# Kernel optimization log

Measured on AMD Instinct MI355X. Metric: run time of the kernel, lower is better.

## Reference

```python
import jax, jax.numpy as jnp
import numpy as np

D = 1024      # embedding_dim
H = 16        # n_heads
HD = D // H   # head_dim = 64
E = 8         # num_experts
K = 2         # top_k
I = 1024      # moe intermediate
S = 2048      # seq_len
B = 1
EPS = 1e-6
THETA = 10000.0


def _rmsnorm(x, w):
    xf = x.astype(jnp.float32)
    var = jnp.mean(xf * xf, axis=-1, keepdims=True)
    return (xf * jax.lax.rsqrt(var + EPS)).astype(x.dtype) * w


def _rope(x, positions):
    # x: [B, S, H, HD], neox-style rotate-half RoPE
    half = HD // 2
    inv_freq = 1.0 / (THETA ** (jnp.arange(0, half, dtype=jnp.float32) / half))
    freqs = positions.astype(jnp.float32)[:, None] * inv_freq[None, :]  # [S, half]
    cos = jnp.cos(freqs)[None, :, None, :]
    sin = jnp.sin(freqs)[None, :, None, :]
    x1, x2 = x[..., :half], x[..., half:]
    return jnp.concatenate([x1 * cos - x2 * sin, x1 * sin + x2 * cos], axis=-1).astype(x.dtype)


def _attn(x, positions, wqkv, wo):
    b, s, _ = x.shape
    qkv = (x @ wqkv).reshape(b, s, 3, H, HD)
    q, k, v = qkv[:, :, 0], qkv[:, :, 1], qkv[:, :, 2]
    q = _rope(q, positions)
    k = _rope(k, positions)
    scale = 1.0 / np.sqrt(HD)
    scores = jnp.einsum('bqhd,bkhd->bhqk', q, k) * scale
    causal = jnp.tril(jnp.ones((s, s), dtype=bool))
    scores = jnp.where(causal[None, None], scores, jnp.finfo(scores.dtype).min)
    probs = jax.nn.softmax(scores, axis=-1)
    o = jnp.einsum('bhqk,bkhd->bqhd', probs, v).reshape(b, s, D)
    return o @ wo


def _moe(x, gate_w, wg, wu, wd):
    # x: [T, D]
    T = x.shape[0]
    logits = x @ gate_w                                    # [T, E]
    probs = jax.nn.softmax(logits.astype(jnp.float32), axis=-1)
    vals, idx = jax.lax.top_k(probs, K)                    # [T, K]
    vals = vals / jnp.sum(vals, axis=-1, keepdims=True)    # renormalize=True
    combine = jnp.zeros((T, E), dtype=jnp.float32)
    combine = combine.at[jnp.arange(T)[:, None], idx].add(vals)
    combine = combine.astype(x.dtype)                      # [T, E]
    out = jnp.zeros_like(x)
    for e in range(E):  # fixed small expert loop; SwiGLU expert FFN
        h = jax.nn.silu(x @ wg[e]) * (x @ wu[e])
        out = out + combine[:, e:e + 1] * (h @ wd[e])
    return out


def setup_inputs() -> dict:
    key = jax.random.key(0)
    ks = jax.random.split(key, 8)
    std = 0.02
    return {
        'positions': jnp.arange(S, dtype=jnp.int32),
        'hidden_states': jax.random.normal(ks[0], (B, S, D), jnp.float32),
        'residual': jax.random.normal(ks[1], (B, S, D), jnp.float32),
        'ln1_w': jnp.ones((D,), jnp.float32),
        'ln2_w': jnp.ones((D,), jnp.float32),
        'wqkv': jax.random.normal(ks[2], (D, 3 * D), jnp.float32) * std,
        'wo': jax.random.normal(ks[3], (D, D), jnp.float32) * std,
        'gate_w': jax.random.normal(ks[4], (D, E), jnp.float32) * std,
        'wg': jax.random.normal(ks[5], (E, D, I), jnp.float32) * std,
        'wu': jax.random.normal(ks[6], (E, D, I), jnp.float32) * std,
        'wd': jax.random.normal(ks[7], (E, I, D), jnp.float32) * std,
    }


def reference(positions, hidden_states, residual, ln1_w, ln2_w, wqkv, wo, gate_w, wg, wu, wd):
    # _forward_with_post_attn_norm: residual arg is overwritten by hidden_states
    res = hidden_states
    x = _rmsnorm(hidden_states, ln1_w)
    x = res + _attn(x, positions, wqkv, wo)
    res2 = x
    y = _rmsnorm(x, ln2_w)
    b, s, _ = y.shape
    moe_out = _moe(y.reshape(-1, D), gate_w, wg, wu, wd).reshape(b, s, D)
    return res2 + moe_out
```

## Files before the change

### kernel.cpp

```cpp
#include <hip/hip_runtime.h>
#include <math.h>

constexpr int S  = 2048;
constexpr int D  = 1024;
constexpr int NH = 16;
constexpr int NE = 8;
constexpr float EPS   = 1e-6f;
constexpr float THETA = 10000.0f;
constexpr float SCL2  = 0.125f * 1.4426950408889634f;
constexpr float LOG2E = 1.4426950408889634f;

typedef unsigned short u16;
typedef unsigned int   u32;
typedef unsigned long long u64;
typedef __attribute__((ext_vector_type(8))) short short8;
typedef __attribute__((ext_vector_type(4))) float f32x4;

__device__ __forceinline__ u16 f2bf(float x) {
  union { float f; u32 u; } v; v.f = x;
  u32 r = (v.u + 0x7FFFu + ((v.u >> 16) & 1u)) >> 16;
  return (u16)r;
}
__device__ __forceinline__ float bf2f(u16 h) {
  union { u32 u; float f; } v; v.u = ((u32)h) << 16;
  return v.f;
}
__device__ __forceinline__ f32x4 mfma16(short8 a, short8 b, f32x4 c) {
  return __builtin_amdgcn_mfma_f32_16x16x32_bf16(a, b, c, 0, 0, 0);
}
__device__ __forceinline__ void gl_lds16(const void* g, void* l) {
  __builtin_amdgcn_global_load_lds((const __attribute__((address_space(1))) u32*)g,
                                   (__attribute__((address_space(3))) u32*)l, 16, 0, 0);
}
__device__ __forceinline__ u64 pack4bf(float a, float b, float c, float d) {
  return (u64)f2bf(a) | ((u64)f2bf(b) << 16) | ((u64)f2bf(c) << 32) | ((u64)f2bf(d) << 48);
}

__global__ __launch_bounds__(256) void prep_kernel(const float* __restrict__ wqkv,
    const float* __restrict__ wo, const float* __restrict__ wg, const float* __restrict__ wu,
    const float* __restrict__ wd, const int* __restrict__ positions,
    const float* __restrict__ hidden, const float* __restrict__ ln1_w,
    u16* __restrict__ wqkvT2, u16* __restrict__ woT2, u16* __restrict__ wgT,
    u16* __restrict__ wuT, u16* __restrict__ wdT, float2* __restrict__ ropetab,
    u16* __restrict__ xn2, int* __restrict__ counts) {
  const int b = blockIdx.x;
  const int tid = threadIdx.x;
  if (b >= 7424) {
    const int t = b - 7424;
    const float* xr = hidden + (size_t)t * D;
    float v[4]; float ss = 0.f;
#pragma unroll
    for (int i = 0; i < 4; ++i) { v[i] = xr[tid + i * 256]; ss += v[i] * v[i]; }
#pragma unroll
    for (int m = 32; m >= 1; m >>= 1) ss += __shfl_xor(ss, m, 64);
    __shared__ float red[4];
    if ((tid & 63) == 0) red[tid >> 6] = ss;
    __syncthreads();
    const float rs = rsqrtf((red[0] + red[1] + red[2] + red[3]) * (1.f / (float)D) + EPS);
#pragma unroll
    for (int i = 0; i < 4; ++i) {
      const int d = tid + i * 256;
      const float y = v[i] * rs * ln1_w[d];
      const u16 h = f2bf(y);
      xn2[(size_t)t * 2048 + d] = h;
      xn2[(size_t)t * 2048 + 1024 + d] = f2bf(y - bf2f(h));
    }
    return;
  }
  if (b >= 7168) {
    if (b == 7168 && tid < 8) counts[tid] = 0;
    const int idx = (b - 7168) * 256 + tid;
    const int t = idx >> 5, p = idx & 31;
    const float inv = powf(THETA, -(float)p * (1.f / 32.f));
    const float fr = (float)positions[t] * inv;
    float sn, cs; sincosf(fr, &sn, &cs);
    ropetab[idx] = make_float2(cs, sn);
    return;
  }
  __shared__ float t_[64][65];
  const float* W; u16* out; int N, n0, k0; bool split;
  if (b < 768) {
    W = wqkv; out = wqkvT2; N = 3072; split = true;
    n0 = (b % 48) * 64; k0 = (b / 48) * 64;
  } else if (b < 1024) {
    W = wo; out = woT2; N = 1024; split = true;
    const int r = b - 768; n0 = (r & 15) * 64; k0 = (r >> 4) * 64;
  } else {
    int r;
    if (b < 3072)      { r = b - 1024; const int e = r >> 8; W = wg + (size_t)e * 1048576; out = wgT + (size_t)e * 1048576; }
    else if (b < 5120) { r = b - 3072; const int e = r >> 8; W = wu + (size_t)e * 1048576; out = wuT + (size_t)e * 1048576; }
    else               { r = b - 5120; const int e = r >> 8; W = wd + (size_t)e * 1048576; out = wdT + (size_t)e * 1048576; }
    N = 1024; split = false;
    r &= 255; n0 = (r & 15) * 64; k0 = (r >> 4) * 64;
  }
  const int rr = tid >> 4, c4 = (tid & 15) * 4;
#pragma unroll
  for (int i = 0; i < 4; ++i) {
    const float4 v = *(const float4*)(W + (size_t)(k0 + rr + i * 16) * N + n0 + c4);
    t_[rr + i * 16][c4 + 0] = v.x; t_[rr + i * 16][c4 + 1] = v.y;
    t_[rr + i * 16][c4 + 2] = v.z; t_[rr + i * 16][c4 + 3] = v.w;
  }
  __syncthreads();
  if (split) {
#pragma unroll
    for (int i = 0; i < 4; ++i) {
      const int n = n0 + rr + i * 16;
      u16* oh = out + (size_t)n * 2048 + k0 + c4;
      const float v0 = t_[c4 + 0][rr + i * 16], v1 = t_[c4 + 1][rr + i * 16];
      const float v2 = t_[c4 + 2][rr + i * 16], v3 = t_[c4 + 3][rr + i * 16];
      *(u64*)(void*)oh = pack4bf(v0, v1, v2, v3);
      *(u64*)(void*)(oh + 1024) = pack4bf(v0 - bf2f(f2bf(v0)), v1 - bf2f(f2bf(v1)),
                                          v2 - bf2f(f2bf(v2)), v3 - bf2f(f2bf(v3)));
    }
  } else {
#pragma unroll
    for (int i = 0; i < 4; ++i) {
      const int n = n0 + rr + i * 16;
      u16* o = out + (size_t)n * 1024 + k0 + c4;
      *(u64*)(void*)o = pack4bf(t_[c4 + 0][rr + i * 16], t_[c4 + 1][rr + i * 16],
                                t_[c4 + 2][rr + i * 16], t_[c4 + 3][rr + i * 16]);
    }
  }
}

__global__ __launch_bounds__(256) void gemm_qkv(const u16* __restrict__ A2,
    const u16* __restrict__ Bt2, float* __restrict__ Cpart) {
  __shared__ u16 As[2][128 * 32];
  __shared__ u16 Bs[2][128 * 32];
  const int b = blockIdx.x;
  const int xcd = b & 7, ii = b >> 3;
  const int m0 = (ii & 15) * 128;
  const int np = (ii >> 4) % 3, ks = (ii >> 4) / 3;
  const int n0 = (xcd * 3 + np) * 128;
  const int kk0 = ks * 48, kk1 = kk0 + 48;
  const int tid = threadIdx.x, wv = tid >> 6, lane = tid & 63;
  const int l15 = lane & 15, lg = lane >> 4;
  const int wr = wv >> 1, wc = wv & 1;
  const int sr = lane >> 2, sk = (lane & 3) * 16;
  const u16* aptr[2]; const u16* bptr[2];
#pragma unroll
  for (int i = 0; i < 2; ++i) {
    aptr[i] = A2 + (size_t)(m0 + (wv * 2 + i) * 16 + sr) * 2048;
    bptr[i] = Bt2 + (size_t)(n0 + (wv * 2 + i) * 16 + sr) * 2048;
  }
  auto STAGE = [&](int buf, int kk) {
    const int t = kk * 32;
    int ka, kb;
    if (t < 1024)      { ka = t;        kb = t; }
    else if (t < 2048) { ka = t;        kb = t - 1024; }
    else               { ka = t - 2048; kb = t - 1024; }
#pragma unroll
    for (int i = 0; i < 2; ++i) {
      gl_lds16((const char*)(aptr[i] + ka) + sk, (char*)As + buf * 8192 + (wv * 2 + i) * 1024);
      gl_lds16((const char*)(bptr[i] + kb) + sk, (char*)Bs + buf * 8192 + (wv * 2 + i) * 1024);
    }
  };
  f32x4 acc[4][4] = {};
  STAGE(0, kk0);
  __syncthreads();
  int cur = 0;
  for (int kk = kk0; kk < kk1; ++kk) {
    if (kk + 1 < kk1) STAGE(cur ^ 1, kk + 1);
    const u16* Ab = (const u16*)As + cur * 4096;
    const u16* Bb = (const u16*)Bs + cur * 4096;
    short8 a[4], bb[4];
#pragma unroll
    for (int i = 0; i < 4; ++i)
      a[i] = *(const short8*)(const void*)(Ab + (size_t)(wr * 64 + i * 16 + l15) * 32 + lg * 8);
#pragma unroll
    for (int j = 0; j < 4; ++j)
      bb[j] = *(const short8*)(const void*)(Bb + (size_t)(wc * 64 + j * 16 + l15) * 32 + lg * 8);
    __builtin_amdgcn_s_setprio(1);
#pragma unroll
    for (int i = 0; i < 4; ++i)
#pragma unroll
      for (int j = 0; j < 4; ++j) acc[i][j] = mfma16(a[i], bb[j], acc[i][j]);
    __builtin_amdgcn_s_setprio(0);
    __syncthreads();
    cur ^= 1;
  }
  float* P = Cpart + (size_t)ks * S * 3072;
#pragma unroll
  for (int i = 0; i < 4; ++i)
#pragma unroll
    for (int j = 0; j < 4; ++j)
#pragma unroll
      for (int r = 0; r < 4; ++r) {
        const int row = m0 + wr * 64 + i * 16 + lg * 4 + r;
        const int col = n0 + wc * 64 + j * 16 + l15;
        P[(size_t)row * 3072 + col] = acc[i][j][r];
      }
}

__global__ __launch_bounds__(256) void qkv_combine(const float* __restrict__ Cp,
    const float2* __restrict__ tab, u16* __restrict__ Ch, u16* __restrict__ Cl) {
  const int t = blockIdx.x, tid = threadIdx.x;
  const float* r0 = Cp + (size_t)t * 3072;
  const float* r1 = r0 + (size_t)S * 3072;
  const size_t ob = (size_t)t * 3072;
#pragma unroll
  for (int i = 0; i < 4; ++i) {
    const int pi = tid + i * 256;
    const int h = pi >> 5, p = pi & 31;
    const int col = h * 64 + p;
    const float x1 = r0[col] + r1[col];
    const float x2 = r0[col + 32] + r1[col + 32];
    const float2 cs = tab[t * 32 + p];
    const float y1 = x1 * cs.x - x2 * cs.y;
    const float y2 = x1 * cs.y + x2 * cs.x;
    const u16 h1 = f2bf(y1);
    Ch[ob + col] = h1; Cl[ob + col] = f2bf(y1 - bf2f(h1));
    const u16 h2 = f2bf(y2);
    Ch[ob + col + 32] = h2; Cl[ob + col + 32] = f2bf(y2 - bf2f(h2));
  }
#pragma unroll
  for (int i = 0; i < 4; ++i) {
    const int col = 2048 + tid + i * 256;
    const float y = r0[col] + r1[col];
    const u16 h = f2bf(y);
    Ch[ob + col] = h; Cl[ob + col] = f2bf(y - bf2f(h));
  }
}

__global__ __launch_bounds__(256) void gemm_wo(const u16* __restrict__ A2,
    const u16* __restrict__ Bt2, float* __restrict__ Pout) {
  constexpr int N = 1024;
  __shared__ u16 As[2][128 * 32];
  __shared__ u16 Bs[2][128 * 32];
  const int b = blockIdx.x;
  const int xcd = b & 7, ii = b >> 3;
  const int n0 = xcd * 128;
  const int m0 = (ii & 15) * 128;
  const int ks = ii >> 4;
  const int kk0 = ks * 24, kk1 = kk0 + 24;
  const int tid = threadIdx.x, wv = tid >> 6, lane = tid & 63;
  const int l15 = lane & 15, lg = lane >> 4;
  const int wr = wv >> 1, wc = wv & 1;
  const int sr = lane >> 2, sk = (lane & 3) * 16;
  const u16* aptr[2]; const u16* bptr[2];
#pragma unroll
  for (int i = 0; i < 2; ++i) {
    aptr[i] = A2 + (size_t)(m0 + (wv * 2 + i) * 16 + sr) * 2048;
    bptr[i] = Bt2 + (size_t)(n0 + (wv * 2 + i) * 16 + sr) * 2048;
  }
  auto STAGE = [&](int buf, int kk) {
    const int t = kk * 32;
    int ka, kb;
    if (t < 1024)      { ka = t;        kb = t; }
    else if (t < 2048) { ka = t;        kb = t - 1024; }
    else               { ka = t - 2048; kb = t - 1024; }
#pragma unroll
    for (int i = 0; i < 2; ++i) {
      gl_lds16((const char*)(aptr[i] + ka) + sk, (char*)As + buf * 8192 + (wv * 2 + i) * 1024);
      gl_lds16((const char*)(bptr[i] + kb) + sk, (char*)Bs + buf * 8192 + (wv * 2 + i) * 1024);
    }
  };
  f32x4 acc[4][4] = {};
  STAGE(0, kk0);
  __syncthreads();
  int cur = 0;
  for (int kk = kk0; kk < kk1; ++kk) {
    if (kk + 1 < kk1) STAGE(cur ^ 1, kk + 1);
    const u16* Ab = (const u16*)As + cur * 4096;
    const u16* Bb = (const u16*)Bs + cur * 4096;
    short8 a[4], bb[4];
#pragma unroll
    for (int i = 0; i < 4; ++i)
      a[i] = *(const short8*)(const void*)(Ab + (size_t)(wr * 64 + i * 16 + l15) * 32 + lg * 8);
#pragma unroll
    for (int j = 0; j < 4; ++j)
      bb[j] = *(const short8*)(const void*)(Bb + (size_t)(wc * 64 + j * 16 + l15) * 32 + lg * 8);
    __builtin_amdgcn_s_setprio(1);
#pragma unroll
    for (int i = 0; i < 4; ++i)
#pragma unroll
      for (int j = 0; j < 4; ++j) acc[i][j] = mfma16(a[i], bb[j], acc[i][j]);
    __builtin_amdgcn_s_setprio(0);
    __syncthreads();
    cur ^= 1;
  }
  float* P = Pout + (size_t)ks * S * N;
#pragma unroll
  for (int i = 0; i < 4; ++i)
#pragma unroll
    for (int j = 0; j < 4; ++j)
#pragma unroll
      for (int r = 0; r < 4; ++r) {
        const int row = m0 + wr * 64 + i * 16 + lg * 4 + r;
        const int col = n0 + wc * 64 + j * 16 + l15;
        P[(size_t)row * N + col] = acc[i][j][r];
      }
}

__global__ __launch_bounds__(256) void attn_mfma(const u16* __restrict__ Qh,
    const u16* __restrict__ Ql, float* __restrict__ Opart, float2* __restrict__ ml) {
  const int b = blockIdx.x;
  const int head = (b & 7) + 8 * ((b >> 3) & 1);
  const int qb = 31 - ((b >> 4) & 31);
  const int sp = (b >> 9) & 3;
  const int q0 = qb * 64;
  const int ktiles = qb + 1;
  const int kbase = ktiles >> 2, krem = ktiles & 3;
  const int t0 = sp * kbase + (sp < krem ? sp : krem);
  const int t1 = t0 + kbase + (sp < krem ? 1 : 0);
  const int tid = threadIdx.x, w = tid >> 6, lane = tid & 63;
  const int l15 = lane & 15, lg = lane >> 4;
  __shared__ u16 Kh[64 * 64];
  __shared__ u16 Kl[64 * 64];
  __shared__ __align__(16) u16 Vth[64 * 72];
  __shared__ __align__(16) u16 Vtl[64 * 72];
  __shared__ u32 Pp[4][16 * 68];

  short8 qh[2], qlo[2];
  {
    const size_t qbase = (size_t)(q0 + w * 16 + l15) * 3072 + head * 64;
    qh[0]  = *(const short8*)(const void*)(Qh + qbase + lg * 8);
    qh[1]  = *(const short8*)(const void*)(Qh + qbase + 32 + lg * 8);
    qlo[0] = *(const short8*)(const void*)(Ql + qbase + lg * 8);
    qlo[1] = *(const short8*)(const void*)(Ql + qbase + 32 + lg * 8);
  }
  f32x4 oacc[4] = {};
  float m_run[4], l_run[4];
#pragma unroll
  for (int r = 0; r < 4; ++r) { m_run[r] = -__builtin_inff(); l_run[r] = 0.f; }
  const int qrow0 = q0 + w * 16 + lg * 4;

  const int vhl = tid >> 7, rem = tid & 127;
  const int vkq = rem & 15, vdg = rem >> 4;
  const u16* vbase = (vhl ? Ql : Qh) + 2048 + head * 64 + vdg * 8;
  u16* vdst = vhl ? Vtl : Vth;
  short8 vr[4];

  auto STAGEK = [&](int kt) {
#pragma unroll
    for (int i = 0; i < 2; ++i) {
      const int inst = w * 2 + i;
      const int key = inst * 8 + (lane >> 3);
      const int db = ((lane & 7) * 16) ^ ((key & 7) << 4);
      gl_lds16((const char*)(Qh + (size_t)(kt * 64 + key) * 3072 + 1024 + head * 64) + db,
               (char*)Kh + inst * 1024);
      gl_lds16((const char*)(Ql + (size_t)(kt * 64 + key) * 3072 + 1024 + head * 64) + db,
               (char*)Kl + inst * 1024);
    }
  };
  auto VLOAD = [&](int kt) {
    const u16* vs = vbase + (size_t)(kt * 64 + vkq * 4) * 3072;
    vr[0] = *(const short8*)(const void*)vs;
    vr[1] = *(const short8*)(const void*)(vs + 3072);
    vr[2] = *(const short8*)(const void*)(vs + 6144);
    vr[3] = *(const short8*)(const void*)(vs + 9216);
  };
  auto VWRITE = [&]() {
#pragma unroll
    for (int jj = 0; jj < 8; ++jj) {
      const u64 pk = (u64)(u16)vr[0][jj] | ((u64)(u16)vr[1][jj] << 16) |
                     ((u64)(u16)vr[2][jj] << 32) | ((u64)(u16)vr[3][jj] << 48);
      *(u64*)(void*)(vdst + (vdg * 8 + jj) * 72 + vkq * 4) = pk;
    }
  };

  if (t0 < t1) {
    STAGEK(t0);
    VLOAD(t0);
    VWRITE();
    __syncthreads();
  }
  for (int t = t0; t < t1; ++t) {
    const int k0 = t * 64;
    const bool more = (t + 1 < t1);
    f32x4 sacc[4];
    __builtin_amdgcn_s_setprio(1);
#pragma unroll
    for (int nt = 0; nt < 4; ++nt) {
      const int key = nt * 16 + l15;
      const char* kbh = (const char*)Kh + key * 128;
      const char* kbl = (const char*)Kl + key * 128;
      const int sw = (key & 7) << 4;
      const short8 kh0 = *(const short8*)(const void*)(kbh + ((lg * 16) ^ sw));
      const short8 kh1 = *(const short8*)(const void*)(kbh + ((64 + lg * 16) ^ sw));
      const short8 kl0 = *(const short8*)(const void*)(kbl + ((lg * 16) ^ sw));
      const short8 kl1 = *(const short8*)(const void*)(kbl + ((64 + lg * 16) ^ sw));
      f32x4 s = {};
      s = mfma16(qh[0], kh0, s); s = mfma16(qh[1], kh1, s);
      s = mfma16(qlo[0], kh0, s); s = mfma16(qlo[1], kh1, s);
      s = mfma16(qh[0], kl0, s); s = mfma16(qh[1], kl1, s);
      sacc[nt] = s;
    }
    __builtin_amdgcn_s_setprio(0);
    __syncthreads();
    if (more) { STAGEK(t + 1); VLOAD(t + 1); }
#pragma unroll
    for (int nt = 0; nt < 4; ++nt)
#pragma unroll
      for (int r = 0; r < 4; ++r) sacc[nt][r] *= SCL2;
    if (t == qb) {
#pragma unroll
      for (int nt = 0; nt < 4; ++nt) {
        const int key = k0 + nt * 16 + l15;
#pragma unroll
        for (int r = 0; r < 4; ++r)
          if (key > qrow0 + r) sacc[nt][r] = -__builtin_inff();
      }
    }
    float mx4[4];
#pragma unroll
    for (int r = 0; r < 4; ++r) {
      float mx = fmaxf(fmaxf(sacc[0][r], sacc[1][r]), fmaxf(sacc[2][r], sacc[3][r]));
#pragma unroll
      for (int msk = 8; msk >= 1; msk >>= 1) mx = fmaxf(mx, __shfl_xor(mx, msk, 64));
      mx4[r] = mx;
    }
    const bool grow = (mx4[0] > m_run[0] + 8.f) || (mx4[1] > m_run[1] + 8.f) ||
                      (mx4[2] > m_run[2] + 8.f) || (mx4[3] > m_run[3] + 8.f);
    if (__any(grow)) {
#pragma unroll
      for (int r = 0; r < 4; ++r) {
        const float m_new = fmaxf(m_run[r], mx4[r]);
        const float fac = __builtin_amdgcn_exp2f(m_run[r] - m_new);
        m_run[r] = m_new;
        l_run[r] *= fac;
#pragma unroll
        for (int nd = 0; nd < 4; ++nd) oacc[nd][r] *= fac;
      }
    }
#pragma unroll
    for (int nt = 0; nt < 4; ++nt)
#pragma unroll
      for (int r = 0; r < 4; ++r)
        sacc[nt][r] = __builtin_amdgcn_exp2f(sacc[nt][r] - m_run[r]);
#pragma unroll
    for (int r = 0; r < 4; ++r) {
      float ls = sacc[0][r] + sacc[1][r] + sacc[2][r] + sacc[3][r];
#pragma unroll
      for (int msk = 8; msk >= 1; msk >>= 1) ls += __shfl_xor(ls, msk, 64);
      l_run[r] += ls;
    }
#pragma unroll
    for (int nt = 0; nt < 4; ++nt)
#pragma unroll
      for (int r = 0; r < 4; ++r) {
        const float p = sacc[nt][r];
        const u32 xu = __float_as_uint(p);
        const u32 hi = xu & 0xFFFF0000u;
        const float pl = p - __uint_as_float(hi);
        const u32 lw = __float_as_uint(pl) >> 16;
        Pp[w][(lg * 4 + r) * 68 + nt * 16 + l15] = (xu >> 16) | (lw << 16);
      }
    __builtin_amdgcn_s_setprio(1);
#pragma unroll
    for (int kk2 = 0; kk2 < 2; ++kk2) {
      const u32* prow = &Pp[w][l15 * 68 + kk2 * 32 + lg * 8];
      const uint4 pq0 = *(const uint4*)prow;
      const uint4 pq1 = *(const uint4*)(prow + 4);
      union U8 { u32 wd[4]; short8 v; } ph_, pl_;
      ph_.wd[0] = (pq0.x & 0xFFFFu) | (pq0.y << 16);
      ph_.wd[1] = (pq0.z & 0xFFFFu) | (pq0.w << 16);
      ph_.wd[2] = (pq1.x & 0xFFFFu) | (pq1.y << 16);
      ph_.wd[3] = (pq1.z & 0xFFFFu) | (pq1.w << 16);
      pl_.wd[0] = (pq0.x >> 16) | (pq0.y & 0xFFFF0000u);
      pl_.wd[1] = (pq0.z >> 16) | (pq0.w & 0xFFFF0000u);
      pl_.wd[2] = (pq1.x >> 16) | (pq1.y & 0xFFFF0000u);
      pl_.wd[3] = (pq1.z >> 16) | (pq1.w & 0xFFFF0000u);
#pragma unroll
      for (int nd = 0; nd < 4; ++nd) {
        const short8 vbh = *(const short8*)(const void*)((const char*)Vth + (nd * 16 + l15) * 144 + kk2 * 64 + lg * 16);
        const short8 vbl = *(const short8*)(const void*)((const char*)Vtl + (nd * 16 + l15) * 144 + kk2 * 64 + lg * 16);
        oacc[nd] = mfma16(ph_.v, vbh, oacc[nd]);
        oacc[nd] = mfma16(pl_.v, vbh, oacc[nd]);
        oacc[nd] = mfma16(ph_.v, vbl, oacc[nd]);
      }
    }
    __builtin_amdgcn_s_setprio(0);
    __syncthreads();
    if (more) VWRITE();
  }
  float* Op = Opart + (size_t)sp * S * 1024;
#pragma unroll
  for (int nd = 0; nd < 4; ++nd)
#pragma unroll
    for (int r = 0; r < 4; ++r)
      Op[(size_t)(qrow0 + r) * 1024 + head * 64 + nd * 16 + l15] = oacc[nd][r];
  if (l15 == 0) {
#pragma unroll
    for (int r = 0; r < 4; ++r)
      ml[((size_t)sp * S + qrow0 + r) * NH + head] = make_float2(m_run[r], l_run[r]);
  }
}

__global__ __launch_bounds__(256) void attn_combine(const float* __restrict__ Op,
    const float2* __restrict__ ml, u16* __restrict__ OA2) {
  const int t = blockIdx.x, tid = threadIdx.x;
  const int h = tid >> 4, dq = (tid & 15) * 4;
  float2 a[4];
  float M = -__builtin_inff();
#pragma unroll
  for (int c = 0; c < 4; ++c) {
    a[c] = ml[((size_t)c * S + t) * NH + h];
    if (a[c].y > 0.f) M = fmaxf(M, a[c].x);
  }
  float e[4], denom = 0.f;
#pragma unroll
  for (int c = 0; c < 4; ++c) {
    e[c] = (a[c].y > 0.f) ? exp2f(a[c].x - M) : 0.f;
    denom += e[c] * a[c].y;
  }
  const float inv = 1.f / denom;
  float ov[4] = {0.f, 0.f, 0.f, 0.f};
#pragma unroll
  for (int c = 0; c < 4; ++c) {
    const float4 v = *(const float4*)(Op + ((size_t)c * S + t) * 1024 + h * 64 + dq);
    ov[0] += e[c] * v.x; ov[1] += e[c] * v.y; ov[2] += e[c] * v.z; ov[3] += e[c] * v.w;
  }
#pragma unroll
  for (int c2 = 0; c2 < 4; ++c2) {
    const float o = ov[c2] * inv;
    const size_t idx = (size_t)t * 2048 + h * 64 + dq + c2;
    const u16 hb = f2bf(o);
    OA2[idx] = hb;
    OA2[idx + 1024] = f2bf(o - bf2f(hb));
  }
}

__global__ __launch_bounds__(256) void rmsnorm_res2_gate(const float* __restrict__ hidden,
    const float* __restrict__ p01, const float* __restrict__ w2, const float* __restrict__ GW,
    float* __restrict__ out, u16* __restrict__ yb,
    int* __restrict__ counts, int* __restrict__ tok_map, float* __restrict__ w_map) {
  const int t = blockIdx.x;
  float v[4]; float ss = 0.f;
#pragma unroll
  for (int i = 0; i < 4; ++i) {
    const size_t idx = (size_t)t * D + threadIdx.x + i * 256;
    const float r = hidden[idx] + p01[idx] + p01[idx + (size_t)S * D] +
                    p01[idx + 2 * (size_t)S * D] + p01[idx + 3 * (size_t)S * D];
    v[i] = r; ss += r * r;
  }
#pragma unroll
  for (int m = 32; m >= 1; m >>= 1) ss += __shfl_xor(ss, m, 64);
  __shared__ float red[4];
  if ((threadIdx.x & 63) == 0) red[threadIdx.x >> 6] = ss;
  __syncthreads();
  const float rs = rsqrtf((red[0] + red[1] + red[2] + red[3]) * (1.f / (float)D) + EPS);
  float lg[8] = {};
#pragma unroll
  for (int i = 0; i < 4; ++i) {
    const int d = threadIdx.x + i * 256;
    const size_t idx = (size_t)t * D + d;
    const float y = v[i] * rs * w2[d];
    out[idx] = v[i];
    yb[idx] = f2bf(y);
    const float4 g0 = *(const float4*)(GW + d * 8);
    const float4 g1 = *(const float4*)(GW + d * 8 + 4);
    lg[0] += y * g0.x; lg[1] += y * g0.y; lg[2] += y * g0.z; lg[3] += y * g0.w;
    lg[4] += y * g1.x; lg[5] += y * g1.y; lg[6] += y * g1.z; lg[7] += y * g1.w;
  }
#pragma unroll
  for (int e = 0; e < 8; ++e)
#pragma unroll
    for (int m = 32; m >= 1; m >>= 1) lg[e] += __shfl_xor(lg[e], m, 64);
  __shared__ float wred[4][8];
  if ((threadIdx.x & 63) == 0)
#pragma unroll
    for (int e = 0; e < 8; ++e) wred[threadIdx.x >> 6][e] = lg[e];
  __syncthreads();
  if (threadIdx.x == 0) {
    float L[8];
#pragma unroll
    for (int e = 0; e < 8; ++e) L[e] = wred[0][e] + wred[1][e] + wred[2][e] + wred[3][e];
    int i0 = 0; float v0 = L[0];
    for (int i = 1; i < 8; ++i) if (L[i] > v0) { v0 = L[i]; i0 = i; }
    int i1 = -1; float v1 = -__builtin_inff();
    for (int i = 0; i < 8; ++i) if (i != i0 && L[i] > v1) { v1 = L[i]; i1 = i; }
    const float e1 = expf(v1 - v0);
    const float inv = 1.f / (1.f + e1);
    const int p0 = atomicAdd(&counts[i0], 1);
    tok_map[i0 * S + p0] = t;
    w_map[i0 * S + p0] = inv;
    const int p1 = atomicAdd(&counts[i1], 1);
    tok_map[i1 * S + p1] = t | 65536;
    w_map[i1 * S + p1] = e1 * inv;
  }
}

__global__ __launch_bounds__(256) void moe_gu(const u16* __restrict__ Yb,
    const u16* __restrict__ Wgb, const u16* __restrict__ Wub, u16* __restrict__ Hb,
    const int* __restrict__ counts, const int* __restrict__ tokmap) {
  const int b = blockIdx.x;
  const int e = b & 7, ii = b >> 3;
  const int n0 = (ii & 15) * 64;
  const int m0 = (ii >> 4) * 128;
  const int cnt = counts[e];
  if (m0 >= cnt) return;
  __shared__ u16 SH[2][16 * 512];
  const int tid = threadIdx.x, wv = tid >> 6, lane = tid & 63;
  const int l15 = lane & 15, lg = lane >> 4;
  const int wr = wv >> 1, wc = wv & 1;
  const int sr = lane >> 2, sk = (lane & 3) * 16;
  const u16* B1 = Wgb + (size_t)e * 1048576;
  const u16* B2 = Wub + (size_t)e * 1048576;
  const u16* cp[4];
#pragma unroll
  for (int i = 0; i < 4; ++i) {
    const int c = wv * 4 + i;
    if (c < 8) {
      const int arow = m0 + c * 16 + sr;
      const int tok = tokmap[e * S + arow] & 2047;
      cp[i] = Yb + (size_t)tok * 1024;
    } else if (c < 12) {
      cp[i] = B1 + (size_t)(n0 + (c - 8) * 16 + sr) * 1024;
    } else {
      cp[i] = B2 + (size_t)(n0 + (c - 12) * 16 + sr) * 1024;
    }
  }
  auto STAGE = [&](int buf, int k) {
#pragma unroll
    for (int i = 0; i < 4; ++i) {
      const int c = wv * 4 + i;
      gl_lds16((const char*)(cp[i] + k) + sk, (char*)SH + buf * 16384 + c * 1024);
    }
  };
  f32x4 acc1[4][2] = {};
  f32x4 acc2[4][2] = {};
  STAGE(0, 0);
  __syncthreads();
  int cur = 0;
  for (int kk = 0; kk < 32; ++kk) {
    if (kk < 31) STAGE(cur ^ 1, (kk + 1) * 32);
    const u16* Sb = (const u16*)SH + cur * 8192;
    short8 a[4], b1f[2], b2f[2];
#pragma unroll
    for (int i = 0; i < 4; ++i)
      a[i] = *(const short8*)(const void*)(Sb + (size_t)(wr * 64 + i * 16 + l15) * 32 + lg * 8);
#pragma unroll
    for (int j = 0; j < 2; ++j) {
      b1f[j] = *(const short8*)(const void*)(Sb + 4096 + (size_t)(wc * 32 + j * 16 + l15) * 32 + lg * 8);
      b2f[j] = *(const short8*)(const void*)(Sb + 6144 + (size_t)(wc * 32 + j * 16 + l15) * 32 + lg * 8);
    }
    __builtin_amdgcn_s_setprio(1);
#pragma unroll
    for (int i = 0; i < 4; ++i)
#pragma unroll
      for (int j = 0; j < 2; ++j) {
        acc1[i][j] = mfma16(a[i], b1f[j], acc1[i][j]);
        acc2[i][j] = mfma16(a[i], b2f[j], acc2[i][j]);
      }
    __builtin_amdgcn_s_setprio(0);
    __syncthreads();
    cur ^= 1;
  }
#pragma unroll
  for (int i = 0; i < 4; ++i)
#pragma unroll
    for (int j = 0; j < 2; ++j)
#pragma unroll
      for (int r = 0; r < 4; ++r) {
        const int row = m0 + wr * 64 + i * 16 + lg * 4 + r;
        if (row < cnt) {
          const float g = acc1[i][j][r];
          const float u = acc2[i][j][r];
          const float sig = __builtin_amdgcn_rcpf(1.f + __builtin_amdgcn_exp2f(-g * LOG2E));
          Hb[((size_t)e * 2048 + row) * 1024 + n0 + wc * 32 + j * 16 + l15] = f2bf(u * g * sig);
        }
      }
}

__global__ __launch_bounds__(256) void moe_down(const u16* __restrict__ Hb,
    const u16* __restrict__ Wdb, u16* __restrict__ slotp,
    const int* __restrict__ counts, const int* __restrict__ tokmap,
    const float* __restrict__ wmap) {
  const int b = blockIdx.x;
  const int e = b & 7, ii = b >> 3;
  const int m0 = (ii & 15) * 128;
  const int n0 = ((ii >> 4) & 7) * 128;
  const int ks = ii >> 7;
  const int cnt = counts[e];
  if (m0 >= cnt) return;
  __shared__ u16 As[2][128 * 32];
  __shared__ u16 Bs[2][128 * 32];
  const int tid = threadIdx.x, wv = tid >> 6, lane = tid & 63;
  const int l15 = lane & 15, lg = lane >> 4;
  const int wr = wv >> 1, wc = wv & 1;
  const int sr = lane >> 2, sk = (lane & 3) * 16;
  const u16* B = Wdb + (size_t)e * 1048576;
  const u16* aptr[2]; const u16* bptr[2];
#pragma unroll
  for (int i = 0; i < 2; ++i) {
    aptr[i] = Hb + ((size_t)e * 2048 + m0 + (wv * 2 + i) * 16 + sr) * 1024;
    bptr[i] = B + (size_t)(n0 + (wv * 2 + i) * 16 + sr) * 1024;
  }
  auto STAGE = [&](int buf, int k) {
#pragma unroll
    for (int i = 0; i < 2; ++i) {
      gl_lds16((const char*)(aptr[i] + k) + sk, (char*)As + buf * 8192 + (wv * 2 + i) * 1024);
      gl_lds16((const char*)(bptr[i] + k) + sk, (char*)Bs + buf * 8192 + (wv * 2 + i) * 1024);
    }
  };
  f32x4 acc[4][4] = {};
  const int kb0 = ks * 16, kb1 = kb0 + 16;
  STAGE(0, kb0 * 32);
  __syncthreads();
  int cur = 0;
  for (int kk = kb0; kk < kb1; ++kk) {
    if (kk + 1 < kb1) STAGE(cur ^ 1, (kk + 1) * 32);
    const u16* Ab = (const u16*)As + cur * 4096;
    const u16* Bb = (const u16*)Bs + cur * 4096;
    short8 a[4], bb[4];
#pragma unroll
    for (int i = 0; i < 4; ++i)
      a[i] = *(const short8*)(const void*)(Ab + (size_t)(wr * 64 + i * 16 + l15) * 32 + lg * 8);
#pragma unroll
    for (int j = 0; j < 4; ++j)
      bb[j] = *(const short8*)(const void*)(Bb + (size_t)(wc * 64 + j * 16 + l15) * 32 + lg * 8);
    __builtin_amdgcn_s_setprio(1);
#pragma unroll
    for (int i = 0; i < 4; ++i)
#pragma unroll
      for (int j = 0; j < 4; ++j) acc[i][j] = mfma16(a[i], bb[j], acc[i][j]);
    __builtin_amdgcn_s_setprio(0);
    __syncthreads();
    cur ^= 1;
  }
#pragma unroll
  for (int i = 0; i < 4; ++i)
#pragma unroll
    for (int j = 0; j < 4; ++j)
#pragma unroll
      for (int r = 0; r < 4; ++r) {
        const int row = m0 + wr * 64 + i * 16 + lg * 4 + r;
        if (row < cnt) {
          const int raw = tokmap[e * S + row];
          const int t = raw & 2047;
          const int sl = (raw >> 16) & 1;
          const float wgt = wmap[e * S + row];
          slotp[((size_t)(sl * 2 + ks) * S + t) * 1024 + n0 + wc * 64 + j * 16 + l15] =
              f2bf(wgt * acc[i][j][r]);
        }
      }
}

__global__ __launch_bounds__(256) void final_add(float* __restrict__ out,
    const u16* __restrict__ sp) {
  const size_t i = ((size_t)blockIdx.x * 256 + threadIdx.x) * 4;
  float4 o = *(float4*)(out + i);
#pragma unroll
  for (int c = 0; c < 4; ++c) {
    const u64 a = *(const u64*)(sp + (size_t)c * S * D + i);
    o.x += bf2f((u16)(a));
    o.y += bf2f((u16)(a >> 16));
    o.z += bf2f((u16)(a >> 32));
    o.w += bf2f((u16)(a >> 48));
  }
  *(float4*)(out + i) = o;
}

extern "C" void kernel_launch(void* const* d_in, const int* in_sizes, int n_in,
                              void* d_out, int out_size, void* d_ws, size_t ws_size,
                              hipStream_t stream) {
  const int*   positions = (const int*)d_in[0];
  const float* hidden    = (const float*)d_in[1];
  const float* ln1_w  = (const float*)d_in[3];
  const float* ln2_w  = (const float*)d_in[4];
  const float* wqkv   = (const float*)d_in[5];
  const float* wo     = (const float*)d_in[6];
  const float* gate_w = (const float*)d_in[7];
  const float* wg     = (const float*)d_in[8];
  const float* wu     = (const float*)d_in[9];
  const float* wd     = (const float*)d_in[10];
  float* out = (float*)d_out;

  char* ws = (char*)d_ws;
  const size_t MB = 1ull << 20;
  u16* wqkvT2 = (u16*)(ws);
  u16* QKVh   = (u16*)(ws);
  u16* OA2    = (u16*)(ws);
  u16* woT2   = (u16*)(ws + 12 * MB);
  u16* wgT    = (u16*)(ws + 16 * MB);
  u16* wuT    = (u16*)(ws + 32 * MB);
  u16* wdT    = (u16*)(ws + 48 * MB);
  float2* ropetab = (float2*)(ws + 64 * MB);
  float2* ml      = (float2*)(ws + 64 * MB + 524288);
  char* mapb = ws + 64 * MB + 1572864;
  int*   counts   = (int*)mapb;
  int*   tok_map  = (int*)(mapb + 8192);
  float* w_map    = (float*)(mapb + 8192 + 65536);
  u16* xn2    = (u16*)(ws + 66 * MB);
  u16* QKVl   = (u16*)(ws + 66 * MB);
  u16* yb     = (u16*)(ws + 66 * MB);
  float* Cpart  = (float*)(ws + 78 * MB);
  float* Opart  = (float*)(ws + 78 * MB);
  float* p01    = (float*)(ws + 78 * MB);
  u16* Hb     = (u16*)(ws + 78 * MB);
  u16* slotp  = (u16*)(ws + 110 * MB);

  prep_kernel<<<9472, 256, 0, stream>>>(wqkv, wo, wg, wu, wd, positions, hidden, ln1_w,
                                        wqkvT2, woT2, wgT, wuT, wdT, ropetab, xn2, counts);
  gemm_qkv<<<768, 256, 0, stream>>>(xn2, wqkvT2, Cpart);
  qkv_combine<<<S, 256, 0, stream>>>(Cpart, ropetab, QKVh, QKVl);
  attn_mfma<<<2048, 256, 0, stream>>>(QKVh, QKVl, Opart, ml);
  attn_combine<<<S, 256, 0, stream>>>(Opart, ml, OA2);
  gemm_wo<<<512, 256, 0, stream>>>(OA2, woT2, p01);
  rmsnorm_res2_gate<<<S, 256, 0, stream>>>(hidden, p01, ln2_w, gate_w, out, yb,
                                           counts, tok_map, w_map);
  moe_gu<<<2048, 256, 0, stream>>>(yb, wgT, wuT, Hb, counts, tok_map);
  moe_down<<<2048, 256, 0, stream>>>(Hb, wdT, slotp, counts, tok_map, w_map);
  final_add<<<2048, 256, 0, stream>>>(out, slotp);
}
```

Before: 315.7 us.

## Transpose attention score MFMA so each lane owns one query row

The QK^T MFMA now uses K as the A operand and Q as B, so each lane holds a single query's scores. Row max and sum then need only two cross-lane shuffles, and the running max and sum shrink to scalars. The Kl tile is no longer staged in LDS; it is read directly from global memory into registers each tile. P is written to LDS as bf16 hi, then rewritten as the lo part for a second PV pass, with launch bounds set to 4 blocks. This is meant to cut shuffle work and LDS footprint, at the cost of uncoalesced global Kl loads and an extra LDS write/read round for P.

```diff
diff --git a/kernel.cpp b/kernel.cpp
--- a/kernel.cpp
+++ b/kernel.cpp
@@ -292,7 +292,7 @@
       }
 }
 
-__global__ __launch_bounds__(256) void attn_mfma(const u16* __restrict__ Qh,
+__global__ __launch_bounds__(256, 4) void attn_mfma(const u16* __restrict__ Qh,
     const u16* __restrict__ Ql, float* __restrict__ Opart, float2* __restrict__ ml) {
   const int b = blockIdx.x;
   const int head = (b & 7) + 8 * ((b >> 3) & 1);
@@ -306,10 +306,9 @@
   const int tid = threadIdx.x, w = tid >> 6, lane = tid & 63;
   const int l15 = lane & 15, lg = lane >> 4;
   __shared__ u16 Kh[64 * 64];
-  __shared__ u16 Kl[64 * 64];
   __shared__ __align__(16) u16 Vth[64 * 72];
   __shared__ __align__(16) u16 Vtl[64 * 72];
-  __shared__ u32 Pp[4][16 * 68];
+  __shared__ __align__(16) u16 Pp[4][16 * 72];
 
   short8 qh[2], qlo[2];
   {
@@ -320,10 +319,9 @@
     qlo[1] = *(const short8*)(const void*)(Ql + qbase + 32 + lg * 8);
   }
   f32x4 oacc[4] = {};
-  float m_run[4], l_run[4];
-#pragma unroll
-  for (int r = 0; r < 4; ++r) { m_run[r] = -__builtin_inff(); l_run[r] = 0.f; }
+  float m_run = -__builtin_inff(), l_run = 0.f;
   const int qrow0 = q0 + w * 16 + lg * 4;
+  const int qcol  = q0 + w * 16 + l15;
 
   const int vhl = tid >> 7, rem = tid & 127;
   const int vkq = rem & 15, vdg = rem >> 4;
@@ -339,8 +337,6 @@
       const int db = ((lane & 7) * 16) ^ ((key & 7) << 4);
       gl_lds16((const char*)(Qh + (size_t)(kt * 64 + key) * 3072 + 1024 + head * 64) + db,
                (char*)Kh + inst * 1024);
-      gl_lds16((const char*)(Ql + (size_t)(kt * 64 + key) * 3072 + 1024 + head * 64) + db,
-               (char*)Kl + inst * 1024);
     }
   };
   auto VLOAD = [&](int kt) {
@@ -368,22 +364,26 @@
   for (int t = t0; t < t1; ++t) {
     const int k0 = t * 64;
     const bool more = (t + 1 < t1);
+    short8 kl[8];
+#pragma unroll
+    for (int nt = 0; nt < 4; ++nt) {
+      const u16* ksrc = Ql + (size_t)(k0 + nt * 16 + l15) * 3072 + 1024 + head * 64 + lg * 8;
+      kl[nt * 2]     = *(const short8*)(const void*)ksrc;
+      kl[nt * 2 + 1] = *(const short8*)(const void*)(ksrc + 32);
+    }
     f32x4 sacc[4];
     __builtin_amdgcn_s_setprio(1);
 #pragma unroll
     for (int nt = 0; nt < 4; ++nt) {
       const int key = nt * 16 + l15;
       const char* kbh = (const char*)Kh + key * 128;
-      const char* kbl = (const char*)Kl + key * 128;
       const int sw = (key & 7) << 4;
       const short8 kh0 = *(const short8*)(const void*)(kbh + ((lg * 16) ^ sw));
       const short8 kh1 = *(const short8*)(const void*)(kbh + ((64 + lg * 16) ^ sw));
-      const short8 kl0 = *(const short8*)(const void*)(kbl + ((lg * 16) ^ sw));
-      const short8 kl1 = *(const short8*)(const void*)(kbl + ((64 + lg * 16) ^ sw));
       f32x4 s = {};
-      s = mfma16(qh[0], kh0, s); s = mfma16(qh[1], kh1, s);
-      s = mfma16(qlo[0], kh0, s); s = mfma16(qlo[1], kh1, s);
-      s = mfma16(qh[0], kl0, s); s = mfma16(qh[1], kl1, s);
+      s = mfma16(kh0, qh[0], s);  s = mfma16(kh1, qh[1], s);
+      s = mfma16(kh0, qlo[0], s); s = mfma16(kh1, qlo[1], s);
+      s = mfma16(kl[nt * 2], qh[0], s); s = mfma16(kl[nt * 2 + 1], qh[1], s);
       sacc[nt] = s;
     }
     __builtin_amdgcn_s_setprio(0);
@@ -396,78 +396,88 @@
     if (t == qb) {
 #pragma unroll
       for (int nt = 0; nt < 4; ++nt) {
-        const int key = k0 + nt * 16 + l15;
+        const int keyb = k0 + nt * 16 + lg * 4;
 #pragma unroll
         for (int r = 0; r < 4; ++r)
-          if (key > qrow0 + r) sacc[nt][r] = -__builtin_inff();
+          if (keyb + r > qcol) sacc[nt][r] = -__builtin_inff();
       }
     }
-    float mx4[4];
-#pragma unroll
-    for (int r = 0; r < 4; ++r) {
-      float mx = fmaxf(fmaxf(sacc[0][r], sacc[1][r]), fmaxf(sacc[2][r], sacc[3][r]));
-#pragma unroll
-      for (int msk = 8; msk >= 1; msk >>= 1) mx = fmaxf(mx, __shfl_xor(mx, msk, 64));
-      mx4[r] = mx;
-    }
-    const bool grow = (mx4[0] > m_run[0] + 8.f) || (mx4[1] > m_run[1] + 8.f) ||
-                      (mx4[2] > m_run[2] + 8.f) || (mx4[3] > m_run[3] + 8.f);
+    float mx = sacc[0][0];
+#pragma unroll
+    for (int nt = 0; nt < 4; ++nt)
+#pragma unroll
+      for (int r = 0; r < 4; ++r) mx = fmaxf(mx, sacc[nt][r]);
+    mx = fmaxf(mx, __shfl_xor(mx, 16, 64));
+    mx = fmaxf(mx, __shfl_xor(mx, 32, 64));
+    const bool grow = mx > m_run + 8.f;
     if (__any(grow)) {
+      const float m_new = fmaxf(m_run, mx);
+      const float fac = __builtin_amdgcn_exp2f(m_run - m_new);
+      m_run = m_new;
+      l_run *= fac;
+      float facB[4];
+#pragma unroll
+      for (int r = 0; r < 4; ++r) facB[r] = __shfl(fac, lg * 4 + r, 64);
+#pragma unroll
+      for (int nd = 0; nd < 4; ++nd)
+#pragma unroll
+        for (int r = 0; r < 4; ++r) oacc[nd][r] *= facB[r];
+    }
+    float ls = 0.f;
+#pragma unroll
+    for (int nt = 0; nt < 4; ++nt)
 #pragma unroll
       for (int r = 0; r < 4; ++r) {
-        const float m_new = fmaxf(m_run[r], mx4[r]);
-        const float fac = __builtin_amdgcn_exp2f(m_run[r] - m_new);
-        m_run[r] = m_new;
-        l_run[r] *= fac;
-#pragma unroll
-        for (int nd = 0; nd < 4; ++nd) oacc[nd][r] *= fac;
+        sacc[nt][r] = __builtin_amdgcn_exp2f(sacc[nt][r] - m_run);
+        ls += sacc[nt][r];
       }
-    }
-#pragma unroll
-    for (int nt = 0; nt < 4; ++nt)
-#pragma unroll
-      for (int r = 0; r < 4; ++r)
-        sacc[nt][r] = __builtin_amdgcn_exp2f(sacc[nt][r] - m_run[r]);
-#pragma unroll
-    for (int r = 0; r < 4; ++r) {
-      float ls = sacc[0][r] + sacc[1][r] + sacc[2][r] + sacc[3][r];
-#pragma unroll
-      for (int msk = 8; msk >= 1; msk >>= 1) ls += __shfl_xor(ls, msk, 64);
-      l_run[r] += ls;
-    }
-#pragma unroll
-    for (int nt = 0; nt < 4; ++nt)
-#pragma unroll
-      for (int r = 0; r < 4; ++r) {
-        const float p = sacc[nt][r];
-        const u32 xu = __float_as_uint(p);
-        const u32 hi = xu & 0xFFFF0000u;
-        const float pl = p - __uint_as_float(hi);
-        const u32 lw = __float_as_uint(pl) >> 16;
-        Pp[w][(lg * 4 + r) * 68 + nt * 16 + l15] = (xu >> 16) | (lw << 16);
-      }
+    ls += __shfl_xor(ls, 16, 64);
+    ls += __shfl_xor(ls, 32, 64);
+    l_run += ls;
+    u16* prow = &Pp[w][l15 * 72];
+#pragma unroll
+    for (int nt = 0; nt < 4; ++nt) {
+      const u64 pk = (u64)(__float_as_uint(sacc[nt][0]) >> 16) |
+                     ((u64)(__float_as_uint(sacc[nt][1]) >> 16) << 16) |
+                     ((u64)(__float_as_uint(sacc[nt][2]) >> 16) << 32) |
+                     ((u64)(__float_as_uint(sacc[nt][3]) >> 16) << 48);
+      *(u64*)(void*)(prow + nt * 16 + lg * 4) = pk;
+    }
     __builtin_amdgcn_s_setprio(1);
 #pragma unroll
     for (int kk2 = 0; kk2 < 2; ++kk2) {
-      const u32* prow = &Pp[w][l15 * 68 + kk2 * 32 + lg * 8];
-      const uint4 pq0 = *(const uint4*)prow;
-      const uint4 pq1 = *(const uint4*)(prow + 4);
-      union U8 { u32 wd[4]; short8 v; } ph_, pl_;
-      ph_.wd[0] = (pq0.x & 0xFFFFu) | (pq0.y << 16);
-      ph_.wd[1] = (pq0.z & 0xFFFFu) | (pq0.w << 16);
-      ph_.wd[2] = (pq1.x & 0xFFFFu) | (pq1.y << 16);
-      ph_.wd[3] = (pq1.z & 0xFFFFu) | (pq1.w << 16);
-      pl_.wd[0] = (pq0.x >> 16) | (pq0.y & 0xFFFF0000u);
-      pl_.wd[1] = (pq0.z >> 16) | (pq0.w & 0xFFFF0000u);
-      pl_.wd[2] = (pq1.x >> 16) | (pq1.y & 0xFFFF0000u);
-      pl_.wd[3] = (pq1.z >> 16) | (pq1.w & 0xFFFF0000u);
+      const short8 pa = *(const short8*)(const void*)((const char*)prow + kk2 * 64 + lg * 16);
 #pragma unroll
       for (int nd = 0; nd < 4; ++nd) {
         const short8 vbh = *(const short8*)(const void*)((const char*)Vth + (nd * 16 + l15) * 144 + kk2 * 64 + lg * 16);
         const short8 vbl = *(const short8*)(const void*)((const char*)Vtl + (nd * 16 + l15) * 144 + kk2 * 64 + lg * 16);
-        oacc[nd] = mfma16(ph_.v, vbh, oacc[nd]);
-        oacc[nd] = mfma16(pl_.v, vbh, oacc[nd]);
-        oacc[nd] = mfma16(ph_.v, vbl, oacc[nd]);
+        oacc[nd] = mfma16(pa, vbh, oacc[nd]);
+        oacc[nd] = mfma16(pa, vbl, oacc[nd]);
+      }
+    }
+    __builtin_amdgcn_s_setprio(0);
+    asm volatile("" ::: "memory");
+#pragma unroll
+    for (int nt = 0; nt < 4; ++nt) {
+      float lo[4];
+#pragma unroll
+      for (int r = 0; r < 4; ++r)
+        lo[r] = sacc[nt][r] - __uint_as_float(__float_as_uint(sacc[nt][r]) & 0xFFFF0000u);
+      const u64 pk = (u64)(__float_as_uint(lo[0]) >> 16) |
+                     ((u64)(__float_as_uint(lo[1]) >> 16) << 16) |
+                     ((u64)(__float_as_uint(lo[2]) >> 16) << 32) |
+                     ((u64)(__float_as_uint(lo[3]) >> 16) << 48);
+      *(u64*)(void*)(prow + nt * 16 + lg * 4) = pk;
+    }
+    asm volatile("" ::: "memory");
+    __builtin_amdgcn_s_setprio(1);
+#pragma unroll
+    for (int kk2 = 0; kk2 < 2; ++kk2) {
+      const short8 pa = *(const short8*)(const void*)((const char*)prow + kk2 * 64 + lg * 16);
+#pragma unroll
+      for (int nd = 0; nd < 4; ++nd) {
+        const short8 vbh = *(const short8*)(const void*)((const char*)Vth + (nd * 16 + l15) * 144 + kk2 * 64 + lg * 16);
+        oacc[nd] = mfma16(pa, vbh, oacc[nd]);
       }
     }
     __builtin_amdgcn_s_setprio(0);
@@ -480,10 +490,8 @@
 #pragma unroll
     for (int r = 0; r < 4; ++r)
       Op[(size_t)(qrow0 + r) * 1024 + head * 64 + nd * 16 + l15] = oacc[nd][r];
-  if (l15 == 0) {
-#pragma unroll
-    for (int r = 0; r < 4; ++r)
-      ml[((size_t)sp * S + qrow0 + r) * NH + head] = make_float2(m_run[r], l_run[r]);
+  if (lg == 0) {
+    ml[((size_t)sp * S + q0 + w * 16 + l15) * NH + head] = make_float2(m_run, l_run);
   }
 }
 
```

After: 326.5 us. 3.4% more time.
